# Kernel optimization log

Hardware: AMD Instinct MI355X
Metric: run time of the kernel (lower is better)

The kernel has to match this reference:

```python
import jax, jax.numpy as jnp
import numpy as np

N = 100000
E = 3200000
F_IN = 165
HIDDEN = 16
N_CLASSES = 2


def setup_inputs() -> dict:
    key = jax.random.key(0)
    k1, k2, k3, k4, k5 = jax.random.split(key, 5)
    x = jax.random.normal(k1, (N, F_IN), dtype=jnp.float32)
    edge_index = jax.random.randint(k2, (2, E), 0, N, dtype=jnp.int64)
    # Glorot-style init for GCNConv weights; biases zero (PyG default)
    W1 = jax.random.normal(k3, (F_IN, HIDDEN), dtype=jnp.float32) / np.sqrt(F_IN)
    b1 = jnp.zeros((HIDDEN,), dtype=jnp.float32)
    W2 = jax.random.normal(k4, (HIDDEN, N_CLASSES), dtype=jnp.float32) / np.sqrt(HIDDEN)
    b2 = jnp.zeros((N_CLASSES,), dtype=jnp.float32)
    return {"x": x, "edge_index": edge_index, "W1": W1, "b1": b1, "W2": W2, "b2": b2}


def _gcn_propagate(h, src, dst, dinv_sqrt, num_nodes):
    """Symmetric-normalized aggregation with implicit self-loops.

    out_i = sum_{j->i} dinv[j]*dinv[i]*h_j + dinv[i]^2 * h_i
    """
    norm = (dinv_sqrt[src] * dinv_sqrt[dst])[:, None]          # [E,1]
    msg = h[src] * norm                                        # [E,D] gather
    agg = jax.ops.segment_sum(msg, dst, num_segments=num_nodes)  # [N,D] scatter
    return agg + h * (dinv_sqrt * dinv_sqrt)[:, None]          # self-loop term


def reference(x, edge_index, W1, b1, W2, b2):
    src = edge_index[0]
    dst = edge_index[1]
    n = x.shape[0]
    # degree with self-loops (edge weight 1), as in PyG gcn_norm
    deg = jax.ops.segment_sum(jnp.ones((src.shape[0],), dtype=x.dtype), dst,
                              num_segments=n) + 1.0
    dinv_sqrt = jax.lax.rsqrt(deg)

    # layer 1: transform -> propagate -> bias -> relu
    h = x @ W1                                                 # [N,16]
    h = _gcn_propagate(h, src, dst, dinv_sqrt, n) + b1
    h = jax.nn.relu(h)

    # layer 2
    h = h @ W2                                                 # [N,2]
    h = _gcn_propagate(h, src, dst, dinv_sqrt, n) + b2

    return jax.nn.log_softmax(h, axis=1)
```

## Files before the change

kernel.cpp:

```cpp
#include <hip/hip_runtime.h>
#include <math.h>

#define F_IN 165
#define HID 16
#define NPB 256
#define NPB_BITS 8
#define MAXB 512
#define CHUNK 4096
#define EPT 16
#define SSTAGE 12288

__device__ __forceinline__ unsigned pk_bf16(float lo, float hi) {
    unsigned a = __float_as_uint(lo), b = __float_as_uint(hi);
    a += 0x7FFF + ((a >> 16) & 1);
    b += 0x7FFF + ((b >> 16) & 1);
    return (a >> 16) | (b & 0xFFFF0000u);
}
#define BF_LO(w) __uint_as_float((w) << 16)
#define BF_HI(w) __uint_as_float((w) & 0xFFFF0000u)

__global__ __launch_bounds__(256) void k_cnt(const int* __restrict__ dst,
                                             int* __restrict__ cbM, int E) {
    __shared__ int h[MAXB];
    int t = threadIdx.x;
    for (int i = t; i < MAXB; i += 256) h[i] = 0;
    __syncthreads();
    int e0 = blockIdx.x * CHUNK;
    int n = min(CHUNK, E - e0);
    if (n == CHUNK) {
        const int4* d4 = (const int4*)(dst + e0);
#pragma unroll
        for (int u = 0; u < 4; ++u) {
            int4 v = d4[u * 256 + t];
            atomicAdd(&h[v.x >> NPB_BITS], 1);
            atomicAdd(&h[v.y >> NPB_BITS], 1);
            atomicAdd(&h[v.z >> NPB_BITS], 1);
            atomicAdd(&h[v.w >> NPB_BITS], 1);
        }
    } else {
        for (int k = t; k < n; k += 256)
            atomicAdd(&h[dst[e0 + k] >> NPB_BITS], 1);
    }
    __syncthreads();
    for (int i = t; i < MAXB; i += 256)
        cbM[blockIdx.x * MAXB + i] = h[i];
}

__global__ __launch_bounds__(256) void k_colscan(int* __restrict__ cbM,
                                                 int* __restrict__ btot, int NB) {
    __shared__ int ps[256];
    int b = blockIdx.x, t = threadIdx.x;
    int i0 = t * 4;
    int v[4];
    int s = 0;
#pragma unroll
    for (int u = 0; u < 4; ++u) {
        int c = i0 + u;
        v[u] = (c < NB) ? cbM[c * MAXB + b] : 0;
        s += v[u];
    }
    ps[t] = s;
    __syncthreads();
    for (int off = 1; off < 256; off <<= 1) {
        int a = (t >= off) ? ps[t - off] : 0;
        __syncthreads();
        ps[t] += a;
        __syncthreads();
    }
    int run = ps[t] - s;
#pragma unroll
    for (int u = 0; u < 4; ++u) {
        int c = i0 + u;
        if (c < NB) cbM[c * MAXB + b] = run;
        run += v[u];
    }
    if (t == 255) btot[b] = ps[255];
}

__global__ __launch_bounds__(256) void k_binscatter(const int* __restrict__ src,
                                                    const int* __restrict__ dst,
                                                    const int* __restrict__ cbM,
                                                    const int* __restrict__ btot,
                                                    unsigned* __restrict__ sedge,
                                                    int E, int nbuck) {
    __shared__ int hist[MAXB];
    __shared__ int lofs[MAXB];
    __shared__ int dlt[MAXB];
    __shared__ int ps[256];
    __shared__ uint2 stg[CHUNK];
    int t = threadIdx.x;
    int me = blockIdx.x;
    int e0 = me * CHUNK;
    int n = min(CHUNK, E - e0);

    int d[EPT], sv[EPT], rk[EPT];
    if (n == CHUNK) {
        const int4* dd = (const int4*)(dst + e0);
        const int4* ss = (const int4*)(src + e0);
#pragma unroll
        for (int u = 0; u < 4; ++u) {
            int4 dv = dd[u * 256 + t];
            int4 vv = ss[u * 256 + t];
            d[u * 4 + 0] = dv.x; d[u * 4 + 1] = dv.y;
            d[u * 4 + 2] = dv.z; d[u * 4 + 3] = dv.w;
            sv[u * 4 + 0] = vv.x; sv[u * 4 + 1] = vv.y;
            sv[u * 4 + 2] = vv.z; sv[u * 4 + 3] = vv.w;
        }
    } else {
#pragma unroll
        for (int u = 0; u < EPT; ++u) {
            int k = t + u * 256;
            d[u]  = (k < n) ? dst[e0 + k] : -1;
            sv[u] = (k < n) ? src[e0 + k] : 0;
        }
    }
    for (int i = t; i < MAXB; i += 256) hist[i] = 0;
    __syncthreads();
#pragma unroll
    for (int u = 0; u < EPT; ++u)
        if (d[u] >= 0) rk[u] = atomicAdd(&hist[d[u] >> NPB_BITS], 1);
    __syncthreads();

    int base = t * 2;
    int h0 = hist[base], h1 = hist[base + 1];
    int s = h0 + h1;
    ps[t] = s;
    __syncthreads();
    for (int off = 1; off < 256; off <<= 1) {
        int a = (t >= off) ? ps[t - off] : 0;
        __syncthreads();
        ps[t] += a;
        __syncthreads();
    }
    int excl = ps[t] - s;
    lofs[base] = excl;
    lofs[base + 1] = excl + h0;

    int c0v = (base < nbuck) ? btot[base] : 0;
    int c1v = (base + 1 < nbuck) ? btot[base + 1] : 0;
    int s2 = c0v + c1v;
    __syncthreads();
    ps[t] = s2;
    __syncthreads();
    for (int off = 1; off < 256; off <<= 1) {
        int a = (t >= off) ? ps[t - off] : 0;
        __syncthreads();
        ps[t] += a;
        __syncthreads();
    }
    int ex2 = ps[t] - s2;
    hist[base] = ex2;
    hist[base + 1] = ex2 + c0v;
    __syncthreads();
    for (int i = t; i < nbuck; i += 256)
        dlt[i] = hist[i] + cbM[me * MAXB + i] - lofs[i];
    __syncthreads();

#pragma unroll
    for (int u = 0; u < EPT; ++u) {
        if (d[u] < 0) continue;
        int b = d[u] >> NPB_BITS;
        int r = lofs[b] + rk[u];
        stg[r] = make_uint2(((unsigned)sv[u] << NPB_BITS) | (unsigned)(d[u] & (NPB - 1)),
                            (unsigned)(dlt[b] + r));
    }
    __syncthreads();

    for (int r = t; r < n; r += 256) {
        uint2 v = stg[r];
        sedge[v.y] = v.x;
    }
}

__global__ __launch_bounds__(256) void k_sortnode(const int* __restrict__ btot,
                                                  const unsigned* __restrict__ sedge,
                                                  int* __restrict__ csr,
                                                  int* __restrict__ rowptr,
                                                  float* __restrict__ dinv,
                                                  int nbuck, int N) {
    __shared__ int hist[256];
    __shared__ int ps[256];
    __shared__ int lcur[256];
    __shared__ int stage[SSTAGE];
    __shared__ int sbase;
    int b = blockIdx.x, t = threadIdx.x;

    int t2 = 2 * t;
    int c0v = (t2 < nbuck) ? btot[t2] : 0;
    int c1v = (t2 + 1 < nbuck) ? btot[t2 + 1] : 0;
    int ssum = c0v + c1v;
    ps[t] = ssum;
    __syncthreads();
    for (int off = 1; off < 256; off <<= 1) {
        int a = (t >= off) ? ps[t - off] : 0;
        __syncthreads();
        ps[t] += a;
        __syncthreads();
    }
    if (t == (b >> 1)) sbase = (ps[t] - ssum) + ((b & 1) ? c0v : 0);
    __syncthreads();
    int base = sbase;
    int n = btot[b];
    if (b == nbuck - 1 && t == 0) rowptr[N] = base + n;

    hist[t] = 0;
    __syncthreads();
    for (int k = t; k < n; k += 256)
        atomicAdd(&hist[sedge[base + k] & (NPB - 1)], 1);
    __syncthreads();
    int c = hist[t];
    ps[t] = c;
    __syncthreads();
    for (int off = 1; off < 256; off <<= 1) {
        int a = (t >= off) ? ps[t - off] : 0;
        __syncthreads();
        ps[t] += a;
        __syncthreads();
    }
    int excl = ps[t] - c;
    int node = b * NPB + t;
    if (node < N) {
        rowptr[node] = base + excl;
        dinv[node] = rsqrtf((float)c + 1.0f);
    }
    lcur[t] = excl;
    __syncthreads();
    bool staged = (n <= SSTAGE);
    for (int k = t; k < n; k += 256) {
        unsigned p = sedge[base + k];
        int dd = p & (NPB - 1);
        int pos = atomicAdd(&lcur[dd], 1);
        int svv = (int)(p >> NPB_BITS);
        if (staged) stage[pos] = svv;
        else        csr[base + pos] = svv;
    }
    __syncthreads();
    if (staged) {
        for (int k = t; k < n; k += 256) csr[base + k] = stage[k];
    }
}

#define FMA1(vv, kk)                                                   \
    {                                                                  \
        float4 w = *(const float4*)(ws + (kk) * HID + c4);             \
        acc.x = fmaf((vv), w.x, acc.x); acc.y = fmaf((vv), w.y, acc.y);\
        acc.z = fmaf((vv), w.z, acc.z); acc.w = fmaf((vv), w.w, acc.w);\
    }

__global__ __launch_bounds__(256) void k_gemm1(const float* __restrict__ x,
                                               const float* __restrict__ W1,
                                               const float* __restrict__ dinv,
                                               unsigned* __restrict__ g1, int N) {
    __shared__ float ws[F_IN * HID];
    int t = threadIdx.x;
    {
        const float4* w4 = (const float4*)W1;
        float4* s4 = (float4*)ws;
#pragma unroll
        for (int u = 0; u < 3; ++u) {
            int i = t + u * 256;
            if (i < (F_IN * HID) / 4) s4[i] = w4[i];
        }
    }
    __syncthreads();
    int gid = blockIdx.x * 256 + t;
    int row = gid >> 2;
    int c4 = (gid & 3) << 2;
    if (row >= N) return;
    const float* xr = x + (long long)row * F_IN;
    float4 acc = make_float4(0.f, 0.f, 0.f, 0.f);

    int p = (4 - (row & 3)) & 3;
    for (int k = 0; k < p; ++k) { float v = xr[k]; FMA1(v, k); }

    const float4* xr4 = (const float4*)(xr + p);
    int n4 = (F_IN - p) >> 2;
    int q = 0;
    for (; q + 4 <= n4; q += 4) {
        float4 v0 = xr4[q], v1 = xr4[q + 1], v2 = xr4[q + 2], v3 = xr4[q + 3];
        int kb = p + q * 4;
        FMA1(v0.x, kb + 0)  FMA1(v0.y, kb + 1)  FMA1(v0.z, kb + 2)  FMA1(v0.w, kb + 3)
        FMA1(v1.x, kb + 4)  FMA1(v1.y, kb + 5)  FMA1(v1.z, kb + 6)  FMA1(v1.w, kb + 7)
        FMA1(v2.x, kb + 8)  FMA1(v2.y, kb + 9)  FMA1(v2.z, kb + 10) FMA1(v2.w, kb + 11)
        FMA1(v3.x, kb + 12) FMA1(v3.y, kb + 13) FMA1(v3.z, kb + 14) FMA1(v3.w, kb + 15)
    }
    for (; q < n4; ++q) {
        float4 v = xr4[q];
        int kb = p + q * 4;
        FMA1(v.x, kb) FMA1(v.y, kb + 1) FMA1(v.z, kb + 2) FMA1(v.w, kb + 3)
    }
    for (int k = p + n4 * 4; k < F_IN; ++k) { float v = xr[k]; FMA1(v, k); }

    float di = dinv[row];
    uint2 o = make_uint2(pk_bf16(acc.x * di, acc.y * di),
                         pk_bf16(acc.z * di, acc.w * di));
    *(uint2*)(g1 + (long long)row * 8 + (gid & 3) * 2) = o;
}

#define ACC8(U)                                                         \
    l0 += BF_LO(U.x); h0 += BF_HI(U.x); l1 += BF_LO(U.y); h1 += BF_HI(U.y); \
    l2 += BF_LO(U.z); h2 += BF_HI(U.z); l3 += BF_LO(U.w); h3 += BF_HI(U.w);

__global__ __launch_bounds__(256) void k_agg1(const int* __restrict__ rowptr,
                                              const int* __restrict__ csr,
                                              const unsigned* __restrict__ g1,
                                              const float* __restrict__ dinv,
                                              const float* __restrict__ b1,
                                              const float* __restrict__ W2,
                                              float* __restrict__ g2, int N) {
    int gid = blockIdx.x * 256 + threadIdx.x;
    int i = gid >> 3;
    int j = gid & 1;
    int part = (gid >> 1) & 3;
    if (i >= N) return;
    int e0 = rowptr[i], e1 = rowptr[i + 1];
    int len = e1 - e0;
    int qs = e0 + ((len * part) >> 2);
    int qe = e0 + ((len * (part + 1)) >> 2);
    const uint4* G = (const uint4*)g1;
    float l0 = 0.f, h0 = 0.f, l1 = 0.f, h1 = 0.f;
    float l2 = 0.f, h2 = 0.f, l3 = 0.f, h3 = 0.f;
    if (part == 0) { uint4 w0 = G[i * 2 + j]; ACC8(w0) }
    int e = qs;
    int p = (4 - (e & 3)) & 3;
    p = min(p, qe - e);
    for (int k = 0; k < p; ++k, ++e) { uint4 u = G[csr[e] * 2 + j]; ACC8(u) }
    const int4* c4 = (const int4*)(csr + e);
    int nq = (qe - e) >> 2;
    int q = 0;
    for (; q + 2 <= nq; q += 2) {
        int4 a = c4[q], b = c4[q + 1];
        uint4 u0 = G[a.x * 2 + j], u1 = G[a.y * 2 + j];
        uint4 u2 = G[a.z * 2 + j], u3 = G[a.w * 2 + j];
        uint4 u4 = G[b.x * 2 + j], u5 = G[b.y * 2 + j];
        uint4 u6 = G[b.z * 2 + j], u7 = G[b.w * 2 + j];
        ACC8(u0) ACC8(u1) ACC8(u2) ACC8(u3)
        ACC8(u4) ACC8(u5) ACC8(u6) ACC8(u7)
    }
    for (; q < nq; ++q) {
        int4 a = c4[q];
        uint4 u0 = G[a.x * 2 + j], u1 = G[a.y * 2 + j];
        uint4 u2 = G[a.z * 2 + j], u3 = G[a.w * 2 + j];
        ACC8(u0) ACC8(u1) ACC8(u2) ACC8(u3)
    }
    e += nq * 4;
    for (; e < qe; ++e) { uint4 u = G[csr[e] * 2 + j]; ACC8(u) }

#pragma unroll
    for (int off = 2; off <= 4; off <<= 1) {
        l0 += __shfl_xor(l0, off, 8); h0 += __shfl_xor(h0, off, 8);
        l1 += __shfl_xor(l1, off, 8); h1 += __shfl_xor(h1, off, 8);
        l2 += __shfl_xor(l2, off, 8); h2 += __shfl_xor(h2, off, 8);
        l3 += __shfl_xor(l3, off, 8); h3 += __shfl_xor(h3, off, 8);
    }
    if (part != 0) return;
    float di = dinv[i];
    int fb = j * 8;
    float c0 = 0.f, c1 = 0.f;
#define EPI(val, fi)                                                     \
    {                                                                    \
        float v = fmaf((val), di, b1[fb + (fi)]);                        \
        v = v > 0.f ? v : 0.f;                                           \
        float2 w = ((const float2*)W2)[fb + (fi)];                       \
        c0 = fmaf(v, w.x, c0);                                           \
        c1 = fmaf(v, w.y, c1);                                           \
    }
    EPI(l0, 0) EPI(h0, 1) EPI(l1, 2) EPI(h1, 3)
    EPI(l2, 4) EPI(h2, 5) EPI(l3, 6) EPI(h3, 7)
    c0 += __shfl_xor(c0, 1, 2);
    c1 += __shfl_xor(c1, 1, 2);
    if (j == 0) ((float2*)g2)[i] = make_float2(c0 * di, c1 * di);
}

__global__ __launch_bounds__(256) void k_agg2(const int* __restrict__ rowptr,
                                              const int* __restrict__ csr,
                                              const float* __restrict__ g2,
                                              const float* __restrict__ dinv,
                                              const float* __restrict__ b2,
                                              float* __restrict__ out, int N) {
    int gid = blockIdx.x * 256 + threadIdx.x;
    int i = gid >> 2;
    int l = gid & 3;
    if (i >= N) return;
    int e0 = rowptr[i], e1 = rowptr[i + 1];
    float a0 = 0.f, a1 = 0.f;
    int e = e0 + l;
    for (; e + 4 < e1; e += 8) {
        int s0 = csr[e], s1 = csr[e + 4];
        float2 u = ((const float2*)g2)[s0];
        float2 w = ((const float2*)g2)[s1];
        a0 += u.x + w.x;
        a1 += u.y + w.y;
    }
    for (; e < e1; e += 4) {
        int s = csr[e];
        float2 u = ((const float2*)g2)[s];
        a0 += u.x;
        a1 += u.y;
    }
    a0 += __shfl_xor(a0, 1, 4); a0 += __shfl_xor(a0, 2, 4);
    a1 += __shfl_xor(a1, 1, 4); a1 += __shfl_xor(a1, 2, 4);
    if (l == 0) {
        float2 self = ((const float2*)g2)[i];
        float di = dinv[i];
        float A = fmaf(a0 + self.x, di, b2[0]);
        float B = fmaf(a1 + self.y, di, b2[1]);
        float m = fmaxf(A, B);
        float lse = m + logf(expf(A - m) + expf(B - m));
        ((float2*)out)[i] = make_float2(A - lse, B - lse);
    }
}

extern "C" void kernel_launch(void* const* d_in, const int* in_sizes, int n_in,
                              void* d_out, int out_size, void* d_ws, size_t ws_size,
                              hipStream_t stream) {
    const float* x  = (const float*)d_in[0];
    const int*   ei = (const int*)d_in[1];
    const float* W1 = (const float*)d_in[2];
    const float* b1 = (const float*)d_in[3];
    const float* W2 = (const float*)d_in[4];
    const float* b2 = (const float*)d_in[5];
    float* out = (float*)d_out;

    int N = in_sizes[0] / F_IN;
    int E = in_sizes[1] / 2;
    const int* src = ei;
    const int* dst = ei + E;
    int nbuck = (N + NPB - 1) >> NPB_BITS;
    int NB = (E + CHUNK - 1) / CHUNK;

    int* cbM      = (int*)d_ws;
    int* btot     = cbM + (long long)NB * MAXB;
    int* rowptr   = btot + MAXB;
    unsigned* sedge = (unsigned*)(rowptr + N + 1);
    int* csr      = (int*)(sedge + E);
    float* dinv   = (float*)(csr + E);
    unsigned* g1  = (unsigned*)(dinv + N);
    float* g2     = (float*)(g1 + (long long)8 * N);

    k_cnt<<<NB, 256, 0, stream>>>(dst, cbM, E);
    k_colscan<<<nbuck, 256, 0, stream>>>(cbM, btot, NB);
    k_binscatter<<<NB, 256, 0, stream>>>(src, dst, cbM, btot, sedge, E, nbuck);
    k_sortnode<<<nbuck, 256, 0, stream>>>(btot, sedge, csr, rowptr, dinv, nbuck, N);

    k_gemm1<<<(N * 4 + 255) / 256, 256, 0, stream>>>(x, W1, dinv, g1, N);

    k_agg1<<<((long long)N * 8 + 255) / 256, 256, 0, stream>>>(rowptr, csr, g1, dinv, b1, W2, g2, N);
    k_agg2<<<(N * 4 + 255) / 256, 256, 0, stream>>>(rowptr, csr, g2, dinv, b2, out, N);
}
```

Before: 122.5 us.

## Fuse GEMM1 with degree counting and apply dinv scaling in sortnode

Merges the feature transform (x@W1) and the destination-bucket counting into one launch by splitting the grid between the two tasks, so the large x read overlaps with the edge histogram instead of waiting for the CSR build. The dinv scaling that used to be applied in the GEMM epilogue is now applied in k_sortnode, which reads back and rewrites each node's bf16 row of g1. This removes a kernel launch and a serial dependency, but adds an extra read and write of g1 and a second bf16 rounding.

Measured after the change: 118.9 us. 2.9% less time.

```diff
diff --git a/kernel.cpp b/kernel.cpp
--- a/kernel.cpp
+++ b/kernel.cpp
@@ -19,31 +19,87 @@
 #define BF_LO(w) __uint_as_float((w) << 16)
 #define BF_HI(w) __uint_as_float((w) & 0xFFFF0000u)
 
-__global__ __launch_bounds__(256) void k_cnt(const int* __restrict__ dst,
-                                             int* __restrict__ cbM, int E) {
-    __shared__ int h[MAXB];
+#define FMA1(vv, kk)                                                   \
+    {                                                                  \
+        float4 w = *(const float4*)(ws + (kk) * HID + c4);             \
+        acc.x = fmaf((vv), w.x, acc.x); acc.y = fmaf((vv), w.y, acc.y);\
+        acc.z = fmaf((vv), w.z, acc.z); acc.w = fmaf((vv), w.w, acc.w);\
+    }
+
+__global__ __launch_bounds__(256) void k_front(const float* __restrict__ x,
+                                               const float* __restrict__ W1,
+                                               unsigned* __restrict__ g1, int N,
+                                               const int* __restrict__ dst,
+                                               int* __restrict__ cbM, int E,
+                                               int NBg) {
     int t = threadIdx.x;
-    for (int i = t; i < MAXB; i += 256) h[i] = 0;
-    __syncthreads();
-    int e0 = blockIdx.x * CHUNK;
-    int n = min(CHUNK, E - e0);
-    if (n == CHUNK) {
-        const int4* d4 = (const int4*)(dst + e0);
-#pragma unroll
-        for (int u = 0; u < 4; ++u) {
-            int4 v = d4[u * 256 + t];
-            atomicAdd(&h[v.x >> NPB_BITS], 1);
-            atomicAdd(&h[v.y >> NPB_BITS], 1);
-            atomicAdd(&h[v.z >> NPB_BITS], 1);
-            atomicAdd(&h[v.w >> NPB_BITS], 1);
+    if ((int)blockIdx.x >= NBg) {
+        __shared__ int h[MAXB];
+        int blk = blockIdx.x - NBg;
+        for (int i = t; i < MAXB; i += 256) h[i] = 0;
+        __syncthreads();
+        int e0 = blk * CHUNK;
+        int n = min(CHUNK, E - e0);
+        if (n == CHUNK) {
+            const int4* d4 = (const int4*)(dst + e0);
+#pragma unroll
+            for (int u = 0; u < 4; ++u) {
+                int4 v = d4[u * 256 + t];
+                atomicAdd(&h[v.x >> NPB_BITS], 1);
+                atomicAdd(&h[v.y >> NPB_BITS], 1);
+                atomicAdd(&h[v.z >> NPB_BITS], 1);
+                atomicAdd(&h[v.w >> NPB_BITS], 1);
+            }
+        } else {
+            for (int k = t; k < n; k += 256)
+                atomicAdd(&h[dst[e0 + k] >> NPB_BITS], 1);
         }
-    } else {
-        for (int k = t; k < n; k += 256)
-            atomicAdd(&h[dst[e0 + k] >> NPB_BITS], 1);
-    }
-    __syncthreads();
-    for (int i = t; i < MAXB; i += 256)
-        cbM[blockIdx.x * MAXB + i] = h[i];
+        __syncthreads();
+        for (int i = t; i < MAXB; i += 256)
+            cbM[blk * MAXB + i] = h[i];
+        return;
+    }
+    __shared__ float ws[F_IN * HID];
+    {
+        const float4* w4 = (const float4*)W1;
+        float4* s4 = (float4*)ws;
+#pragma unroll
+        for (int u = 0; u < 3; ++u) {
+            int i = t + u * 256;
+            if (i < (F_IN * HID) / 4) s4[i] = w4[i];
+        }
+    }
+    __syncthreads();
+    int gid = blockIdx.x * 256 + t;
+    int row = gid >> 2;
+    int c4 = (gid & 3) << 2;
+    if (row >= N) return;
+    const float* xr = x + (long long)row * F_IN;
+    float4 acc = make_float4(0.f, 0.f, 0.f, 0.f);
+
+    int p = (4 - (row & 3)) & 3;
+    for (int k = 0; k < p; ++k) { float v = xr[k]; FMA1(v, k); }
+
+    const float4* xr4 = (const float4*)(xr + p);
+    int n4 = (F_IN - p) >> 2;
+    int q = 0;
+    for (; q + 4 <= n4; q += 4) {
+        float4 v0 = xr4[q], v1 = xr4[q + 1], v2 = xr4[q + 2], v3 = xr4[q + 3];
+        int kb = p + q * 4;
+        FMA1(v0.x, kb + 0)  FMA1(v0.y, kb + 1)  FMA1(v0.z, kb + 2)  FMA1(v0.w, kb + 3)
+        FMA1(v1.x, kb + 4)  FMA1(v1.y, kb + 5)  FMA1(v1.z, kb + 6)  FMA1(v1.w, kb + 7)
+        FMA1(v2.x, kb + 8)  FMA1(v2.y, kb + 9)  FMA1(v2.z, kb + 10) FMA1(v2.w, kb + 11)
+        FMA1(v3.x, kb + 12) FMA1(v3.y, kb + 13) FMA1(v3.z, kb + 14) FMA1(v3.w, kb + 15)
+    }
+    for (; q < n4; ++q) {
+        float4 v = xr4[q];
+        int kb = p + q * 4;
+        FMA1(v.x, kb) FMA1(v.y, kb + 1) FMA1(v.z, kb + 2) FMA1(v.w, kb + 3)
+    }
+    for (int k = p + n4 * 4; k < F_IN; ++k) { float v = xr[k]; FMA1(v, k); }
+
+    uint2 o = make_uint2(pk_bf16(acc.x, acc.y), pk_bf16(acc.z, acc.w));
+    *(uint2*)(g1 + (long long)row * 8 + (gid & 3) * 2) = o;
 }
 
 __global__ __launch_bounds__(256) void k_colscan(int* __restrict__ cbM,
@@ -177,6 +233,7 @@
                                                   int* __restrict__ csr,
                                                   int* __restrict__ rowptr,
                                                   float* __restrict__ dinv,
+                                                  unsigned* __restrict__ g1,
                                                   int nbuck, int N) {
     __shared__ int hist[256];
     __shared__ int ps[256];
@@ -221,7 +278,19 @@
     int node = b * NPB + t;
     if (node < N) {
         rowptr[node] = base + excl;
-        dinv[node] = rsqrtf((float)c + 1.0f);
+        float di = rsqrtf((float)c + 1.0f);
+        dinv[node] = di;
+        uint4* gr = (uint4*)(g1 + (long long)node * 8);
+        uint4 a = gr[0], bb = gr[1];
+        a.x = pk_bf16(BF_LO(a.x) * di, BF_HI(a.x) * di);
+        a.y = pk_bf16(BF_LO(a.y) * di, BF_HI(a.y) * di);
+        a.z = pk_bf16(BF_LO(a.z) * di, BF_HI(a.z) * di);
+        a.w = pk_bf16(BF_LO(a.w) * di, BF_HI(a.w) * di);
+        bb.x = pk_bf16(BF_LO(bb.x) * di, BF_HI(bb.x) * di);
+        bb.y = pk_bf16(BF_LO(bb.y) * di, BF_HI(bb.y) * di);
+        bb.z = pk_bf16(BF_LO(bb.z) * di, BF_HI(bb.z) * di);
+        bb.w = pk_bf16(BF_LO(bb.w) * di, BF_HI(bb.w) * di);
+        gr[0] = a; gr[1] = bb;
     }
     lcur[t] = excl;
     __syncthreads();
@@ -238,63 +307,6 @@
     if (staged) {
         for (int k = t; k < n; k += 256) csr[base + k] = stage[k];
     }
-}
-
-#define FMA1(vv, kk)                                                   \
-    {                                                                  \
-        float4 w = *(const float4*)(ws + (kk) * HID + c4);             \
-        acc.x = fmaf((vv), w.x, acc.x); acc.y = fmaf((vv), w.y, acc.y);\
-        acc.z = fmaf((vv), w.z, acc.z); acc.w = fmaf((vv), w.w, acc.w);\
-    }
-
-__global__ __launch_bounds__(256) void k_gemm1(const float* __restrict__ x,
-                                               const float* __restrict__ W1,
-                                               const float* __restrict__ dinv,
-                                               unsigned* __restrict__ g1, int N) {
-    __shared__ float ws[F_IN * HID];
-    int t = threadIdx.x;
-    {
-        const float4* w4 = (const float4*)W1;
-        float4* s4 = (float4*)ws;
-#pragma unroll
-        for (int u = 0; u < 3; ++u) {
-            int i = t + u * 256;
-            if (i < (F_IN * HID) / 4) s4[i] = w4[i];
-        }
-    }
-    __syncthreads();
-    int gid = blockIdx.x * 256 + t;
-    int row = gid >> 2;
-    int c4 = (gid & 3) << 2;
-    if (row >= N) return;
-    const float* xr = x + (long long)row * F_IN;
-    float4 acc = make_float4(0.f, 0.f, 0.f, 0.f);
-
-    int p = (4 - (row & 3)) & 3;
-    for (int k = 0; k < p; ++k) { float v = xr[k]; FMA1(v, k); }
-
-    const float4* xr4 = (const float4*)(xr + p);
-    int n4 = (F_IN - p) >> 2;
-    int q = 0;
-    for (; q + 4 <= n4; q += 4) {
-        float4 v0 = xr4[q], v1 = xr4[q + 1], v2 = xr4[q + 2], v3 = xr4[q + 3];
-        int kb = p + q * 4;
-        FMA1(v0.x, kb + 0)  FMA1(v0.y, kb + 1)  FMA1(v0.z, kb + 2)  FMA1(v0.w, kb + 3)
-        FMA1(v1.x, kb + 4)  FMA1(v1.y, kb + 5)  FMA1(v1.z, kb + 6)  FMA1(v1.w, kb + 7)
-        FMA1(v2.x, kb + 8)  FMA1(v2.y, kb + 9)  FMA1(v2.z, kb + 10) FMA1(v2.w, kb + 11)
-        FMA1(v3.x, kb + 12) FMA1(v3.y, kb + 13) FMA1(v3.z, kb + 14) FMA1(v3.w, kb + 15)
-    }
-    for (; q < n4; ++q) {
-        float4 v = xr4[q];
-        int kb = p + q * 4;
-        FMA1(v.x, kb) FMA1(v.y, kb + 1) FMA1(v.z, kb + 2) FMA1(v.w, kb + 3)
-    }
-    for (int k = p + n4 * 4; k < F_IN; ++k) { float v = xr[k]; FMA1(v, k); }
-
-    float di = dinv[row];
-    uint2 o = make_uint2(pk_bf16(acc.x * di, acc.y * di),
-                         pk_bf16(acc.z * di, acc.w * di));
-    *(uint2*)(g1 + (long long)row * 8 + (gid & 3) * 2) = o;
 }
 
 #define ACC8(U)                                                         \
@@ -428,6 +440,7 @@
     const int* dst = ei + E;
     int nbuck = (N + NPB - 1) >> NPB_BITS;
     int NB = (E + CHUNK - 1) / CHUNK;
+    int NBg = (N * 4 + 255) / 256;
 
     int* cbM      = (int*)d_ws;
     int* btot     = cbM + (long long)NB * MAXB;
@@ -438,12 +451,10 @@
     unsigned* g1  = (unsigned*)(dinv + N);
     float* g2     = (float*)(g1 + (long long)8 * N);
 
-    k_cnt<<<NB, 256, 0, stream>>>(dst, cbM, E);
+    k_front<<<NBg + NB, 256, 0, stream>>>(x, W1, g1, N, dst, cbM, E, NBg);
     k_colscan<<<nbuck, 256, 0, stream>>>(cbM, btot, NB);
     k_binscatter<<<NB, 256, 0, stream>>>(src, dst, cbM, btot, sedge, E, nbuck);
-    k_sortnode<<<nbuck, 256, 0, stream>>>(btot, sedge, csr, rowptr, dinv, nbuck, N);
-
-    k_gemm1<<<(N * 4 + 255) / 256, 256, 0, stream>>>(x, W1, dinv, g1, N);
+    k_sortnode<<<nbuck, 256, 0, stream>>>(btot, sedge, csr, rowptr, dinv, g1, nbuck, N);
 
     k_agg1<<<((long long)N * 8 + 255) / 256, 256, 0, stream>>>(rowptr, csr, g1, dinv, b1, W2, g2, N);
     k_agg2<<<(N * 4 + 255) / 256, 256, 0, stream>>>(rowptr, csr, g2, dinv, b2, out, N);
```
